# Optimization experiments

Measured on AMD Instinct MI355X. Metric: run time of the kernel, lower is better.

## Reference

```python
import jax, jax.numpy as jnp
import numpy as np
import math

B, LC, LQ, D = 64, 1024, 128, 128


def setup_inputs() -> dict:
    key = jax.random.key(0)
    k1, k2, k3, k4, k5 = jax.random.split(key, 5)
    c_rep = jax.random.normal(k1, (B, LC, D), dtype=jnp.float32)
    q_rep = jax.random.normal(k2, (B, LQ, D), dtype=jnp.float32)
    c_mask = jax.random.randint(k3, (B, LC), 0, 2, dtype=jnp.int32)
    q_mask = jax.random.randint(k4, (B, LQ), 0, 2, dtype=jnp.int32)
    lim = math.sqrt(1.0 / D)
    w = jax.random.uniform(k5, (3 * D,), dtype=jnp.float32, minval=-lim, maxval=lim)
    return {"c_rep": c_rep, "q_rep": q_rep, "c_mask": c_mask, "q_mask": q_mask, "w": w}


def _mask_logits(t, m):
    # mask == 1 means masked (matches original: target*(1-mask) + mask*-1e30)
    return t * (1.0 - m) + m * (-1e30)


def reference(c_rep, q_rep, c_mask, q_mask, w):
    d = c_rep.shape[-1]
    w1, w2, w3 = w[:d], w[d:2 * d], w[2 * d:]
    # Trilinear similarity S[b,i,j] = <ct,w1> + <qt,w2> + <ct*qt,w3>
    # computed without materializing the [B,Lc,Lq,3D] concat tensor.
    S = (c_rep @ w1)[:, :, None] \
        + (q_rep @ w2)[:, None, :] \
        + jnp.einsum('bid,bjd->bij', c_rep * w3, q_rep)  # [B, Lc, Lq]
    qm = q_mask[:, None, :].astype(S.dtype)  # [B, 1, Lq]
    cm = c_mask[:, :, None].astype(S.dtype)  # [B, Lc, 1]
    S1 = jax.nn.softmax(_mask_logits(S, qm), axis=2)  # softmax over query dim
    S2 = jax.nn.softmax(_mask_logits(S, cm), axis=1)  # softmax over context dim
    A = jnp.einsum('bij,bjd->bid', S1, q_rep)  # [B, Lc, D]
    # B_att = S1 @ S2^T @ c_rep, associated right-first to avoid [B,Lc,Lc]
    T = jnp.einsum('bkj,bkd->bjd', S2, c_rep)  # [B, Lq, D]
    B_att = jnp.einsum('bij,bjd->bid', S1, T)  # [B, Lc, D]
    out = jnp.concatenate([c_rep, A, c_rep * A, c_rep * B_att], axis=2)  # [B, Lc, 4D]
    # dropout is identity at inference
    return out
```

## Files before the change

kernel.cpp:

```cpp
#include <hip/hip_runtime.h>
#include <hip/hip_bf16.h>
#include <cstdint>
#include <cstddef>

#define B_   64
#define LC_  1024
#define LQ_  128
#define D_   128

typedef __bf16 bf16;
typedef bf16  bf16x8 __attribute__((ext_vector_type(8)));
typedef bf16  bf16x4 __attribute__((ext_vector_type(4)));
typedef float f32x4  __attribute__((ext_vector_type(4)));

__device__ __forceinline__ f32x4 mfma16(bf16x8 a, bf16x8 b, f32x4 c) {
  return __builtin_amdgcn_mfma_f32_16x16x32_bf16(a, b, c, 0, 0, 0);
}

__global__ __launch_bounds__(256) void k0c(const float* __restrict__ c, const float* __restrict__ w,
                                           float* __restrict__ cw1, bf16* __restrict__ cw3,
                                           bf16* __restrict__ cT) {
  __shared__ float w1s[128];
  __shared__ float w3s[128];
  __shared__ bf16  ctile[128 * 132];
  const int b = blockIdx.y, ks = blockIdx.x;
  const int k0 = ks * 128;
  const int t = threadIdx.x;
  if (t < 128) { w1s[t] = w[t]; w3s[t] = w[256 + t]; }
  __syncthreads();
  {
    const int r = t >> 1, d0 = (t & 1) * 64;
    const float* crow = c + ((size_t)(b * LC_ + k0 + r) * D_ + d0);
    bf16* orow = cw3 + ((size_t)(b * LC_ + k0 + r) * D_ + d0);
    float dot = 0.f;
#pragma unroll
    for (int v = 0; v < 8; ++v) {
      const float4 f0 = ((const float4*)crow)[v * 2 + 0];
      const float4 f1 = ((const float4*)crow)[v * 2 + 1];
      const int dd = d0 + v * 8;
      dot += f0.x * w1s[dd + 0] + f0.y * w1s[dd + 1] + f0.z * w1s[dd + 2] + f0.w * w1s[dd + 3]
           + f1.x * w1s[dd + 4] + f1.y * w1s[dd + 5] + f1.z * w1s[dd + 6] + f1.w * w1s[dd + 7];
      bf16* cr = &ctile[r * 132 + dd];
      cr[0] = (bf16)f0.x; cr[1] = (bf16)f0.y; cr[2] = (bf16)f0.z; cr[3] = (bf16)f0.w;
      cr[4] = (bf16)f1.x; cr[5] = (bf16)f1.y; cr[6] = (bf16)f1.z; cr[7] = (bf16)f1.w;
      bf16x8 o;
      o[0] = (bf16)(f0.x * w3s[dd + 0]); o[1] = (bf16)(f0.y * w3s[dd + 1]);
      o[2] = (bf16)(f0.z * w3s[dd + 2]); o[3] = (bf16)(f0.w * w3s[dd + 3]);
      o[4] = (bf16)(f1.x * w3s[dd + 4]); o[5] = (bf16)(f1.y * w3s[dd + 5]);
      o[6] = (bf16)(f1.z * w3s[dd + 6]); o[7] = (bf16)(f1.w * w3s[dd + 7]);
      *(bf16x8*)(orow + v * 8) = o;
    }
    dot += __shfl_xor(dot, 1);
    if ((t & 1) == 0) cw1[b * LC_ + k0 + r] = dot;
  }
  __syncthreads();
  {
    const int d = t >> 1, kh = (t & 1) * 64;
    bf16* trow = cT + ((size_t)(b * D_ + d) * LC_ + k0 + kh);
#pragma unroll
    for (int v = 0; v < 8; ++v) {
      bf16x8 o;
#pragma unroll
      for (int e = 0; e < 8; ++e) o[e] = ctile[(kh + v * 8 + e) * 132 + d];
      *(bf16x8*)(trow + v * 8) = o;
    }
  }
}

__global__ __launch_bounds__(256) void k0q(const float* __restrict__ q, const float* __restrict__ w,
                                           float* __restrict__ qw2, bf16* __restrict__ qb,
                                           bf16* __restrict__ qT) {
  __shared__ float w2s[128];
  __shared__ bf16  qtile[128 * 132];
  const int b = blockIdx.x;
  const int t = threadIdx.x;
  if (t < 128) w2s[t] = w[128 + t];
  __syncthreads();
  {
    const int r = t >> 1, d0 = (t & 1) * 64;
    const float* qrow = q + ((size_t)(b * LQ_ + r) * D_ + d0);
    bf16* orow = qb + ((size_t)(b * LQ_ + r) * D_ + d0);
    float dot = 0.f;
#pragma unroll
    for (int v = 0; v < 8; ++v) {
      const float4 f0 = ((const float4*)qrow)[v * 2 + 0];
      const float4 f1 = ((const float4*)qrow)[v * 2 + 1];
      const int dd = d0 + v * 8;
      dot += f0.x * w2s[dd + 0] + f0.y * w2s[dd + 1] + f0.z * w2s[dd + 2] + f0.w * w2s[dd + 3]
           + f1.x * w2s[dd + 4] + f1.y * w2s[dd + 5] + f1.z * w2s[dd + 6] + f1.w * w2s[dd + 7];
      bf16x8 o;
      o[0] = (bf16)f0.x; o[1] = (bf16)f0.y; o[2] = (bf16)f0.z; o[3] = (bf16)f0.w;
      o[4] = (bf16)f1.x; o[5] = (bf16)f1.y; o[6] = (bf16)f1.z; o[7] = (bf16)f1.w;
      bf16* qr = &qtile[r * 132 + dd];
#pragma unroll
      for (int e = 0; e < 8; ++e) qr[e] = o[e];
      *(bf16x8*)(orow + v * 8) = o;
    }
    dot += __shfl_xor(dot, 1);
    if ((t & 1) == 0) qw2[b * LQ_ + r] = dot;
  }
  __syncthreads();
  {
    const int d = t >> 1, jh = (t & 1) * 64;
    bf16* trow = qT + ((size_t)(b * D_ + d) * LQ_ + jh);
#pragma unroll
    for (int v = 0; v < 8; ++v) {
      bf16x8 o;
#pragma unroll
      for (int e = 0; e < 8; ++e) o[e] = qtile[(jh + v * 8 + e) * 132 + d];
      *(bf16x8*)(trow + v * 8) = o;
    }
  }
}

__global__ __launch_bounds__(512) void k1p(const float* __restrict__ cw1, const float* __restrict__ qw2,
                                           const int* __restrict__ cmask,
                                           const bf16* __restrict__ cw3, const bf16* __restrict__ cT,
                                           const bf16* __restrict__ qb,
                                           float* __restrict__ Tpart, float* __restrict__ lpart) {
  __shared__ bf16  qs[128 * 136];
  __shared__ bf16  cw3t[64 * 136];
  __shared__ bf16  cTt[128 * 72];
  __shared__ bf16  PT[128 * 72];
  __shared__ float lred[4][128];
  const int ks = blockIdx.x, b = blockIdx.y;
  const int t = threadIdx.x;
  const int w = t >> 6, lane = t & 63, quad = lane >> 4, l15 = lane & 15;
  const int wk = w >> 1, wj = w & 1;

#pragma unroll
  for (int idx = t; idx < 2048; idx += 512) {
    const int row = idx >> 4, ch = idx & 15;
    *(bf16x8*)&qs[row * 136 + ch * 8] =
        *(const bf16x8*)(qb + ((size_t)(b * LQ_ + row) * D_ + ch * 8));
  }
  const f32x4 z = {0.f, 0.f, 0.f, 0.f};
  f32x4 Tacc[4][2];
#pragma unroll
  for (int jt = 0; jt < 4; ++jt) { Tacc[jt][0] = z; Tacc[jt][1] = z; }
  float lacc[4] = {0.f, 0.f, 0.f, 0.f};
  float qv[4];
#pragma unroll
  for (int jt = 0; jt < 4; ++jt) qv[jt] = qw2[b * LQ_ + wj * 64 + jt * 16 + l15];
  __syncthreads();

  for (int kt = 0; kt < 4; ++kt) {
    const int k0g = ks * 256 + kt * 64;
#pragma unroll
    for (int idx = t; idx < 1024; idx += 512) {
      const int row = idx >> 4, ch = idx & 15;
      *(bf16x8*)&cw3t[row * 136 + ch * 8] =
          *(const bf16x8*)(cw3 + ((size_t)(b * LC_ + k0g + row) * D_ + ch * 8));
    }
#pragma unroll
    for (int idx = t; idx < 1024; idx += 512) {
      const int row = idx >> 3, ch = idx & 7;
      *(bf16x8*)&cTt[row * 72 + ch * 8] =
          *(const bf16x8*)(cT + ((size_t)(b * D_ + row) * LC_ + k0g + ch * 8));
    }
    __syncthreads();

    f32x4 S[4] = {z, z, z, z};
#pragma unroll
    for (int kk = 0; kk < 4; ++kk) {
      bf16x8 a = *(bf16x8*)&cw3t[(wk * 16 + l15) * 136 + kk * 32 + quad * 8];
#pragma unroll
      for (int jt = 0; jt < 4; ++jt) {
        bf16x8 bq = *(bf16x8*)&qs[(wj * 64 + jt * 16 + l15) * 136 + kk * 32 + quad * 8];
        S[jt] = mfma16(a, bq, S[jt]);
      }
    }
#pragma unroll
    for (int jt = 0; jt < 4; ++jt) {
      bf16x4 pk;
#pragma unroll
      for (int rr = 0; rr < 4; ++rr) {
        const int krow = k0g + wk * 16 + quad * 4 + rr;
        const float c1 = cw1[b * LC_ + krow];
        const int   cm = cmask[b * LC_ + krow];
        const float p = cm ? 0.f : __expf(S[jt][rr] + c1 + qv[jt]);
        lacc[jt] += p;
        pk[rr] = (bf16)p;
      }
      *(bf16x4*)&PT[(wj * 64 + jt * 16 + l15) * 72 + wk * 16 + quad * 4] = pk;
    }
    __syncthreads();

#pragma unroll
    for (int kk = 0; kk < 2; ++kk) {
      bf16x8 bd0 = *(bf16x8*)&cTt[(wk * 32 + l15) * 72 + kk * 32 + quad * 8];
      bf16x8 bd1 = *(bf16x8*)&cTt[(wk * 32 + 16 + l15) * 72 + kk * 32 + quad * 8];
#pragma unroll
      for (int jt = 0; jt < 4; ++jt) {
        bf16x8 aP = *(bf16x8*)&PT[(wj * 64 + jt * 16 + l15) * 72 + kk * 32 + quad * 8];
        Tacc[jt][0] = mfma16(aP, bd0, Tacc[jt][0]);
        Tacc[jt][1] = mfma16(aP, bd1, Tacc[jt][1]);
      }
    }
    __syncthreads();
  }

#pragma unroll
  for (int jt = 0; jt < 4; ++jt) {
    lacc[jt] += __shfl_xor(lacc[jt], 16);
    lacc[jt] += __shfl_xor(lacc[jt], 32);
  }
  if (lane < 16) {
#pragma unroll
    for (int jt = 0; jt < 4; ++jt) lred[wk][wj * 64 + jt * 16 + l15] = lacc[jt];
  }
  __syncthreads();
  if (t < 128)
    lpart[(size_t)(b * 4 + ks) * 128 + t] =
        lred[0][t] + lred[1][t] + lred[2][t] + lred[3][t];

  float* tp = Tpart + ((size_t)(b * 4 + ks)) * (128 * 128);
#pragma unroll
  for (int jt = 0; jt < 4; ++jt)
#pragma unroll
    for (int dt = 0; dt < 2; ++dt)
#pragma unroll
      for (int rr = 0; rr < 4; ++rr)
        tp[(wj * 64 + jt * 16 + quad * 4 + rr) * 128 + wk * 32 + dt * 16 + l15] =
            Tacc[jt][dt][rr];
}

__global__ __launch_bounds__(256) void k1r(const float* __restrict__ Tpart,
                                           const float* __restrict__ lpart,
                                           bf16* __restrict__ TT) {
  __shared__ float Tsum[32 * 132];
  __shared__ float linv[32];
  const int js = blockIdx.x, b = blockIdx.y;
  const int j0 = js * 32;
  const int t = threadIdx.x;
  const float4* p0 = (const float4*)(Tpart + ((size_t)(b * 4 + 0)) * (128 * 128)) + j0 * 32;
  const float4* p1 = (const float4*)(Tpart + ((size_t)(b * 4 + 1)) * (128 * 128)) + j0 * 32;
  const float4* p2 = (const float4*)(Tpart + ((size_t)(b * 4 + 2)) * (128 * 128)) + j0 * 32;
  const float4* p3 = (const float4*)(Tpart + ((size_t)(b * 4 + 3)) * (128 * 128)) + j0 * 32;
#pragma unroll
  for (int idx = t; idx < 1024; idx += 256) {
    const int row = idx >> 5, seg = idx & 31;
    const float4 v0 = p0[idx];
    const float4 v1 = p1[idx];
    const float4 v2 = p2[idx];
    const float4 v3 = p3[idx];
    float4 s;
    s.x = v0.x + v1.x + v2.x + v3.x;
    s.y = v0.y + v1.y + v2.y + v3.y;
    s.z = v0.z + v1.z + v2.z + v3.z;
    s.w = v0.w + v1.w + v2.w + v3.w;
    *(float4*)&Tsum[row * 132 + seg * 4] = s;
  }
  if (t < 32)
    linv[t] = 1.f / (lpart[(size_t)(b * 4 + 0) * 128 + j0 + t] +
                     lpart[(size_t)(b * 4 + 1) * 128 + j0 + t] +
                     lpart[(size_t)(b * 4 + 2) * 128 + j0 + t] +
                     lpart[(size_t)(b * 4 + 3) * 128 + j0 + t]);
  __syncthreads();
  const int d = t >> 1, jh = (t & 1) * 16;
  bf16x8 o0, o1;
#pragma unroll
  for (int e = 0; e < 8; ++e) {
    o0[e] = (bf16)(Tsum[(jh + e) * 132 + d] * linv[jh + e]);
    o1[e] = (bf16)(Tsum[(jh + 8 + e) * 132 + d] * linv[jh + 8 + e]);
  }
  bf16* dst = TT + ((size_t)(b * D_ + d) * LQ_ + j0 + jh);
  *(bf16x8*)dst = o0;
  *(bf16x8*)(dst + 8) = o1;
}

__global__ __launch_bounds__(256) void k2(const float* __restrict__ c, const float* __restrict__ cw1,
                                          const float* __restrict__ qw2, const int* __restrict__ qmask,
                                          const bf16* __restrict__ cw3, const bf16* __restrict__ qb,
                                          const bf16* __restrict__ qT, const bf16* __restrict__ TT,
                                          float* __restrict__ out) {
  __shared__ __align__(16) char smem[51712];
  bf16* cw3i = (bf16*)(smem);
  bf16* qsl  = (bf16*)(smem + 17408);
  bf16* qTsl = (bf16*)(smem + 26112);
  bf16* TTsl = (bf16*)(smem + 36352);
  bf16* P1   = (bf16*)(smem + 46592);
  float* A32 = (float*)(smem);
  float* B32 = (float*)(smem + 16896);
  const int it = blockIdx.x, b = blockIdx.y;
  const int i0 = it * 64;
  const int t = threadIdx.x;
  const int w = t >> 6, lane = t & 63, quad = lane >> 4, l15 = lane & 15;

#pragma unroll
  for (int idx = t; idx < 1024; idx += 256) {
    const int row = idx >> 4, ch = idx & 15;
    *(bf16x8*)&cw3i[row * 136 + ch * 8] =
        *(const bf16x8*)(cw3 + ((size_t)(b * LC_ + i0 + row) * D_ + ch * 8));
  }
  const f32x4 z = {0.f, 0.f, 0.f, 0.f};
  f32x4 Aacc[8], Bacc[8];
#pragma unroll
  for (int n = 0; n < 8; ++n) { Aacc[n] = z; Bacc[n] = z; }
  float lacc[4] = {0.f, 0.f, 0.f, 0.f};
  __syncthreads();

  for (int jt = 0; jt < 4; ++jt) {
    const int j0 = jt * 32;
#pragma unroll
    for (int idx = t; idx < 512; idx += 256) {
      const int row = idx >> 4, ch = idx & 15;
      *(bf16x8*)&qsl[row * 136 + ch * 8] =
          *(const bf16x8*)(qb + ((size_t)(b * LQ_ + j0 + row) * D_ + ch * 8));
    }
#pragma unroll
    for (int idx = t; idx < 512; idx += 256) {
      const int row = idx >> 2, ch = idx & 3;
      *(bf16x8*)&qTsl[row * 40 + ch * 8] =
          *(const bf16x8*)(qT + ((size_t)(b * D_ + row) * LQ_ + j0 + ch * 8));
    }
#pragma unroll
    for (int idx = t; idx < 512; idx += 256) {
      const int row = idx >> 2, ch = idx & 3;
      *(bf16x8*)&TTsl[row * 40 + ch * 8] =
          *(const bf16x8*)(TT + ((size_t)(b * D_ + row) * LQ_ + j0 + ch * 8));
    }
    __syncthreads();

    f32x4 S0 = z, S1 = z;
#pragma unroll
    for (int kk = 0; kk < 4; ++kk) {
      bf16x8 a  = *(bf16x8*)&cw3i[(w * 16 + l15) * 136 + kk * 32 + quad * 8];
      bf16x8 b0 = *(bf16x8*)&qsl[l15 * 136 + kk * 32 + quad * 8];
      bf16x8 b1 = *(bf16x8*)&qsl[(16 + l15) * 136 + kk * 32 + quad * 8];
      S0 = mfma16(a, b0, S0);
      S1 = mfma16(a, b1, S1);
    }
    const float qv0 = qw2[b * LQ_ + j0 + l15];
    const float qv1 = qw2[b * LQ_ + j0 + 16 + l15];
    const int   qm0 = qmask[b * LQ_ + j0 + l15];
    const int   qm1 = qmask[b * LQ_ + j0 + 16 + l15];
#pragma unroll
    for (int rr = 0; rr < 4; ++rr) {
      const int irow = i0 + w * 16 + quad * 4 + rr;
      const float c1 = cw1[b * LC_ + irow];
      const float p0 = qm0 ? 0.f : __expf(S0[rr] + c1 + qv0);
      const float p1 = qm1 ? 0.f : __expf(S1[rr] + c1 + qv1);
      lacc[rr] += p0 + p1;
      P1[(w * 16 + quad * 4 + rr) * 40 + l15] = (bf16)p0;
      P1[(w * 16 + quad * 4 + rr) * 40 + 16 + l15] = (bf16)p1;
    }
    __syncthreads();

    bf16x8 aP = *(bf16x8*)&P1[(w * 16 + l15) * 40 + quad * 8];
#pragma unroll
    for (int nt = 0; nt < 8; ++nt) {
      bf16x8 bq = *(bf16x8*)&qTsl[(nt * 16 + l15) * 40 + quad * 8];
      bf16x8 bt = *(bf16x8*)&TTsl[(nt * 16 + l15) * 40 + quad * 8];
      Aacc[nt] = mfma16(aP, bq, Aacc[nt]);
      Bacc[nt] = mfma16(aP, bt, Bacc[nt]);
    }
    __syncthreads();
  }

#pragma unroll
  for (int rr = 0; rr < 4; ++rr) {
    float v = lacc[rr];
    v += __shfl_xor(v, 1); v += __shfl_xor(v, 2);
    v += __shfl_xor(v, 4); v += __shfl_xor(v, 8);
    lacc[rr] = 1.f / v;
  }

#pragma unroll
  for (int h = 0; h < 2; ++h) {
    if ((w >> 1) == h) {
      const int lrow0 = (w & 1) * 16 + quad * 4;
#pragma unroll
      for (int nt = 0; nt < 8; ++nt)
#pragma unroll
        for (int rr = 0; rr < 4; ++rr) {
          A32[(lrow0 + rr) * 132 + nt * 16 + l15] = Aacc[nt][rr] * lacc[rr];
          B32[(lrow0 + rr) * 132 + nt * 16 + l15] = Bacc[nt][rr] * lacc[rr];
        }
    }
    __syncthreads();
#pragma unroll
    for (int idx = t; idx < 1024; idx += 256) {
      const int lrow = idx >> 5, seg = idx & 31;
      const size_t grow = (size_t)(b * LC_ + i0 + h * 32 + lrow);
      const float4 c4 = ((const float4*)(c + grow * D_))[seg];
      const float4 a4 = *(float4*)&A32[lrow * 132 + seg * 4];
      const float4 b4 = *(float4*)&B32[lrow * 132 + seg * 4];
      float4* ob = (float4*)(out + grow * 512);
      ob[seg] = c4;
      ob[32 + seg] = a4;
      float4 ca; ca.x = c4.x * a4.x; ca.y = c4.y * a4.y; ca.z = c4.z * a4.z; ca.w = c4.w * a4.w;
      ob[64 + seg] = ca;
      float4 cb; cb.x = c4.x * b4.x; cb.y = c4.y * b4.y; cb.z = c4.z * b4.z; cb.w = c4.w * b4.w;
      ob[96 + seg] = cb;
    }
    __syncthreads();
  }
}

extern "C" void kernel_launch(void* const* d_in, const int* in_sizes, int n_in,
                              void* d_out, int out_size, void* d_ws, size_t ws_size,
                              hipStream_t stream) {
  (void)in_sizes; (void)n_in; (void)out_size; (void)ws_size;
  const float* c     = (const float*)d_in[0];
  const float* q     = (const float*)d_in[1];
  const int*   cmask = (const int*)d_in[2];
  const int*   qmask = (const int*)d_in[3];
  const float* w     = (const float*)d_in[4];
  float* out = (float*)d_out;

  char* ws = (char*)d_ws;
  float* cw1 = (float*)(ws + 0);
  float* qw2 = (float*)(ws + 262144);
  bf16*  cw3 = (bf16*)(ws + 294912);
  bf16*  cT  = (bf16*)(ws + 17072128);
  bf16*  qb  = (bf16*)(ws + 33849344);
  bf16*  qT  = (bf16*)(ws + 35946496);
  bf16*  TT  = (bf16*)(ws + 38043648);

  float* Tpart = out;
  float* lpart = out + 4194304;

  k0c<<<dim3(8, 64), 256, 0, stream>>>(c, w, cw1, cw3, cT);
  k0q<<<dim3(64), 256, 0, stream>>>(q, w, qw2, qb, qT);
  k1p<<<dim3(4, 64), 512, 0, stream>>>(cw1, qw2, cmask, cw3, cT, qb, Tpart, lpart);
  k1r<<<dim3(4, 64), 256, 0, stream>>>(Tpart, lpart, TT);
  k2<<<dim3(16, 64), 256, 0, stream>>>(c, cw1, qw2, qmask, cw3, qb, qT, TT, out);
}
```

Before: 237.7 us.

## Split k1p finer and load MFMA operands directly from global memory

k1p now runs on 16x64 blocks of 256 threads. Each block covers a 128-row context slice and a 64-query half, and the 8 partials are then reduced in k1r. The cw3/cT tiles in k1p and the q/qT/TT tiles in k2 are no longer staged through LDS; MFMA fragments are read straight from global memory, and the remaining LDS arrays use XOR swizzling in place of padding. The aim is to raise occupancy and parallelism and to remove LDS copies and barriers, at the cost of more global/L2 traffic, uncoalesced fragment loads, and a larger partial-sum buffer.

After: 265.9 us. 11.9% more time.

```diff
diff --git a/kernel.cpp b/kernel.cpp
--- a/kernel.cpp
+++ b/kernel.cpp
@@ -16,6 +16,8 @@
 __device__ __forceinline__ f32x4 mfma16(bf16x8 a, bf16x8 b, f32x4 c) {
   return __builtin_amdgcn_mfma_f32_16x16x32_bf16(a, b, c, 0, 0, 0);
 }
+
+__device__ __forceinline__ int swz(int row, int elem) { return elem ^ ((row & 7) << 3); }
 
 __global__ __launch_bounds__(256) void k0c(const float* __restrict__ c, const float* __restrict__ w,
                                            float* __restrict__ cw1, bf16* __restrict__ cw3,
@@ -113,26 +115,26 @@
   }
 }
 
-__global__ __launch_bounds__(512) void k1p(const float* __restrict__ cw1, const float* __restrict__ qw2,
+__global__ __launch_bounds__(256) void k1p(const float* __restrict__ cw1, const float* __restrict__ qw2,
                                            const int* __restrict__ cmask,
                                            const bf16* __restrict__ cw3, const bf16* __restrict__ cT,
                                            const bf16* __restrict__ qb,
                                            float* __restrict__ Tpart, float* __restrict__ lpart) {
-  __shared__ bf16  qs[128 * 136];
-  __shared__ bf16  cw3t[64 * 136];
-  __shared__ bf16  cTt[128 * 72];
-  __shared__ bf16  PT[128 * 72];
-  __shared__ float lred[4][128];
-  const int ks = blockIdx.x, b = blockIdx.y;
+  __shared__ bf16  qs[64 * 128];
+  __shared__ bf16  PT[64 * 64];
+  __shared__ float lred[4][64];
+  const int bx = blockIdx.x;
+  const int ks = bx >> 1, jh = bx & 1;
+  const int b = blockIdx.y;
+  const int j0g = jh * 64;
   const int t = threadIdx.x;
-  const int w = t >> 6, lane = t & 63, quad = lane >> 4, l15 = lane & 15;
-  const int wk = w >> 1, wj = w & 1;
-
-#pragma unroll
-  for (int idx = t; idx < 2048; idx += 512) {
+  const int wk = t >> 6, lane = t & 63, quad = lane >> 4, l15 = lane & 15;
+
+#pragma unroll
+  for (int idx = t; idx < 1024; idx += 256) {
     const int row = idx >> 4, ch = idx & 15;
-    *(bf16x8*)&qs[row * 136 + ch * 8] =
-        *(const bf16x8*)(qb + ((size_t)(b * LQ_ + row) * D_ + ch * 8));
+    *(bf16x8*)&qs[row * 128 + swz(row, ch * 8)] =
+        *(const bf16x8*)(qb + ((size_t)(b * LQ_ + j0g + row) * D_ + ch * 8));
   }
   const f32x4 z = {0.f, 0.f, 0.f, 0.f};
   f32x4 Tacc[4][2];
@@ -141,58 +143,55 @@
   float lacc[4] = {0.f, 0.f, 0.f, 0.f};
   float qv[4];
 #pragma unroll
-  for (int jt = 0; jt < 4; ++jt) qv[jt] = qw2[b * LQ_ + wj * 64 + jt * 16 + l15];
-  __syncthreads();
-
-  for (int kt = 0; kt < 4; ++kt) {
-    const int k0g = ks * 256 + kt * 64;
-#pragma unroll
-    for (int idx = t; idx < 1024; idx += 512) {
-      const int row = idx >> 4, ch = idx & 15;
-      *(bf16x8*)&cw3t[row * 136 + ch * 8] =
-          *(const bf16x8*)(cw3 + ((size_t)(b * LC_ + k0g + row) * D_ + ch * 8));
-    }
-#pragma unroll
-    for (int idx = t; idx < 1024; idx += 512) {
-      const int row = idx >> 3, ch = idx & 7;
-      *(bf16x8*)&cTt[row * 72 + ch * 8] =
-          *(const bf16x8*)(cT + ((size_t)(b * D_ + row) * LC_ + k0g + ch * 8));
-    }
-    __syncthreads();
+  for (int jt = 0; jt < 4; ++jt) qv[jt] = qw2[b * LQ_ + j0g + jt * 16 + l15];
+  __syncthreads();
+
+  for (int kt = 0; kt < 2; ++kt) {
+    const int k0g = ks * 128 + kt * 64;
 
     f32x4 S[4] = {z, z, z, z};
 #pragma unroll
     for (int kk = 0; kk < 4; ++kk) {
-      bf16x8 a = *(bf16x8*)&cw3t[(wk * 16 + l15) * 136 + kk * 32 + quad * 8];
+      const bf16x8 a = *(const bf16x8*)(cw3 +
+          ((size_t)(b * LC_ + k0g + wk * 16 + l15) * D_ + kk * 32 + quad * 8));
 #pragma unroll
       for (int jt = 0; jt < 4; ++jt) {
-        bf16x8 bq = *(bf16x8*)&qs[(wj * 64 + jt * 16 + l15) * 136 + kk * 32 + quad * 8];
+        const int jr = jt * 16 + l15;
+        const bf16x8 bq = *(const bf16x8*)&qs[jr * 128 + swz(jr, kk * 32 + quad * 8)];
         S[jt] = mfma16(a, bq, S[jt]);
       }
     }
+    float c1v[4]; int cmv[4];
+#pragma unroll
+    for (int rr = 0; rr < 4; ++rr) {
+      const int krow = k0g + wk * 16 + quad * 4 + rr;
+      c1v[rr] = cw1[b * LC_ + krow];
+      cmv[rr] = cmask[b * LC_ + krow];
+    }
 #pragma unroll
     for (int jt = 0; jt < 4; ++jt) {
       bf16x4 pk;
 #pragma unroll
       for (int rr = 0; rr < 4; ++rr) {
-        const int krow = k0g + wk * 16 + quad * 4 + rr;
-        const float c1 = cw1[b * LC_ + krow];
-        const int   cm = cmask[b * LC_ + krow];
-        const float p = cm ? 0.f : __expf(S[jt][rr] + c1 + qv[jt]);
+        const float p = cmv[rr] ? 0.f : __expf(S[jt][rr] + c1v[rr] + qv[jt]);
         lacc[jt] += p;
         pk[rr] = (bf16)p;
       }
-      *(bf16x4*)&PT[(wj * 64 + jt * 16 + l15) * 72 + wk * 16 + quad * 4] = pk;
+      const int jr = jt * 16 + l15;
+      *(bf16x4*)&PT[jr * 64 + swz(jr, wk * 16 + quad * 4)] = pk;
     }
     __syncthreads();
 
 #pragma unroll
     for (int kk = 0; kk < 2; ++kk) {
-      bf16x8 bd0 = *(bf16x8*)&cTt[(wk * 32 + l15) * 72 + kk * 32 + quad * 8];
-      bf16x8 bd1 = *(bf16x8*)&cTt[(wk * 32 + 16 + l15) * 72 + kk * 32 + quad * 8];
+      const bf16x8 bd0 = *(const bf16x8*)(cT +
+          ((size_t)(b * D_ + wk * 32 + l15) * LC_ + k0g + kk * 32 + quad * 8));
+      const bf16x8 bd1 = *(const bf16x8*)(cT +
+          ((size_t)(b * D_ + wk * 32 + 16 + l15) * LC_ + k0g + kk * 32 + quad * 8));
 #pragma unroll
       for (int jt = 0; jt < 4; ++jt) {
-        bf16x8 aP = *(bf16x8*)&PT[(wj * 64 + jt * 16 + l15) * 72 + kk * 32 + quad * 8];
+        const int jr = jt * 16 + l15;
+        const bf16x8 aP = *(const bf16x8*)&PT[jr * 64 + swz(jr, kk * 32 + quad * 8)];
         Tacc[jt][0] = mfma16(aP, bd0, Tacc[jt][0]);
         Tacc[jt][1] = mfma16(aP, bd1, Tacc[jt][1]);
       }
@@ -207,21 +206,21 @@
   }
   if (lane < 16) {
 #pragma unroll
-    for (int jt = 0; jt < 4; ++jt) lred[wk][wj * 64 + jt * 16 + l15] = lacc[jt];
-  }
-  __syncthreads();
-  if (t < 128)
-    lpart[(size_t)(b * 4 + ks) * 128 + t] =
+    for (int jt = 0; jt < 4; ++jt) lred[wk][jt * 16 + l15] = lacc[jt];
+  }
+  __syncthreads();
+  if (t < 64)
+    lpart[(size_t)(b * 8 + ks) * 128 + j0g + t] =
         lred[0][t] + lred[1][t] + lred[2][t] + lred[3][t];
 
-  float* tp = Tpart + ((size_t)(b * 4 + ks)) * (128 * 128);
+  float* tp = Tpart + ((size_t)(b * 8 + ks)) * (128 * 128);
 #pragma unroll
   for (int jt = 0; jt < 4; ++jt)
 #pragma unroll
     for (int dt = 0; dt < 2; ++dt)
 #pragma unroll
       for (int rr = 0; rr < 4; ++rr)
-        tp[(wj * 64 + jt * 16 + quad * 4 + rr) * 128 + wk * 32 + dt * 16 + l15] =
+        tp[(j0g + jt * 16 + quad * 4 + rr) * 128 + wk * 32 + dt * 16 + l15] =
             Tacc[jt][dt][rr];
 }
 
@@ -233,38 +232,32 @@
   const int js = blockIdx.x, b = blockIdx.y;
   const int j0 = js * 32;
   const int t = threadIdx.x;
-  const float4* p0 = (const float4*)(Tpart + ((size_t)(b * 4 + 0)) * (128 * 128)) + j0 * 32;
-  const float4* p1 = (const float4*)(Tpart + ((size_t)(b * 4 + 1)) * (128 * 128)) + j0 * 32;
-  const float4* p2 = (const float4*)(Tpart + ((size_t)(b * 4 + 2)) * (128 * 128)) + j0 * 32;
-  const float4* p3 = (const float4*)(Tpart + ((size_t)(b * 4 + 3)) * (128 * 128)) + j0 * 32;
 #pragma unroll
   for (int idx = t; idx < 1024; idx += 256) {
     const int row = idx >> 5, seg = idx & 31;
-    const float4 v0 = p0[idx];
-    const float4 v1 = p1[idx];
-    const float4 v2 = p2[idx];
-    const float4 v3 = p3[idx];
-    float4 s;
-    s.x = v0.x + v1.x + v2.x + v3.x;
-    s.y = v0.y + v1.y + v2.y + v3.y;
-    s.z = v0.z + v1.z + v2.z + v3.z;
-    s.w = v0.w + v1.w + v2.w + v3.w;
+    float4 s = {0.f, 0.f, 0.f, 0.f};
+#pragma unroll
+    for (int i = 0; i < 8; ++i) {
+      const float4 v = ((const float4*)(Tpart + ((size_t)(b * 8 + i)) * (128 * 128)) + j0 * 32)[idx];
+      s.x += v.x; s.y += v.y; s.z += v.z; s.w += v.w;
+    }
     *(float4*)&Tsum[row * 132 + seg * 4] = s;
   }
-  if (t < 32)
-    linv[t] = 1.f / (lpart[(size_t)(b * 4 + 0) * 128 + j0 + t] +
-                     lpart[(size_t)(b * 4 + 1) * 128 + j0 + t] +
-                     lpart[(size_t)(b * 4 + 2) * 128 + j0 + t] +
-                     lpart[(size_t)(b * 4 + 3) * 128 + j0 + t]);
-  __syncthreads();
-  const int d = t >> 1, jh = (t & 1) * 16;
+  if (t < 32) {
+    float l = 0.f;
+#pragma unroll
+    for (int i = 0; i < 8; ++i) l += lpart[(size_t)(b * 8 + i) * 128 + j0 + t];
+    linv[t] = 1.f / l;
+  }
+  __syncthreads();
+  const int d = t >> 1, jhh = (t & 1) * 16;
   bf16x8 o0, o1;
 #pragma unroll
   for (int e = 0; e < 8; ++e) {
-    o0[e] = (bf16)(Tsum[(jh + e) * 132 + d] * linv[jh + e]);
-    o1[e] = (bf16)(Tsum[(jh + 8 + e) * 132 + d] * linv[jh + 8 + e]);
-  }
-  bf16* dst = TT + ((size_t)(b * D_ + d) * LQ_ + j0 + jh);
+    o0[e] = (bf16)(Tsum[(jhh + e) * 132 + d] * linv[jhh + e]);
+    o1[e] = (bf16)(Tsum[(jhh + 8 + e) * 132 + d] * linv[jhh + 8 + e]);
+  }
+  bf16* dst = TT + ((size_t)(b * D_ + d) * LQ_ + j0 + jhh);
   *(bf16x8*)dst = o0;
   *(bf16x8*)(dst + 8) = o1;
 }
@@ -274,12 +267,8 @@
                                           const bf16* __restrict__ cw3, const bf16* __restrict__ qb,
                                           const bf16* __restrict__ qT, const bf16* __restrict__ TT,
                                           float* __restrict__ out) {
-  __shared__ __align__(16) char smem[51712];
-  bf16* cw3i = (bf16*)(smem);
-  bf16* qsl  = (bf16*)(smem + 17408);
-  bf16* qTsl = (bf16*)(smem + 26112);
-  bf16* TTsl = (bf16*)(smem + 36352);
-  bf16* P1   = (bf16*)(smem + 46592);
+  __shared__ __align__(16) char smem[33792];
+  bf16* P1   = (bf16*)(smem);
   float* A32 = (float*)(smem);
   float* B32 = (float*)(smem + 16896);
   const int it = blockIdx.x, b = blockIdx.y;
@@ -287,49 +276,29 @@
   const int t = threadIdx.x;
   const int w = t >> 6, lane = t & 63, quad = lane >> 4, l15 = lane & 15;
 
-#pragma unroll
-  for (int idx = t; idx < 1024; idx += 256) {
-    const int row = idx >> 4, ch = idx & 15;
-    *(bf16x8*)&cw3i[row * 136 + ch * 8] =
-        *(const bf16x8*)(cw3 + ((size_t)(b * LC_ + i0 + row) * D_ + ch * 8));
-  }
+  bf16x8 aF[4];
+#pragma unroll
+  for (int kk = 0; kk < 4; ++kk)
+    aF[kk] = *(const bf16x8*)(cw3 +
+        ((size_t)(b * LC_ + i0 + w * 16 + l15) * D_ + kk * 32 + quad * 8));
+
   const f32x4 z = {0.f, 0.f, 0.f, 0.f};
   f32x4 Aacc[8], Bacc[8];
 #pragma unroll
   for (int n = 0; n < 8; ++n) { Aacc[n] = z; Bacc[n] = z; }
   float lacc[4] = {0.f, 0.f, 0.f, 0.f};
-  __syncthreads();
 
   for (int jt = 0; jt < 4; ++jt) {
     const int j0 = jt * 32;
-#pragma unroll
-    for (int idx = t; idx < 512; idx += 256) {
-      const int row = idx >> 4, ch = idx & 15;
-      *(bf16x8*)&qsl[row * 136 + ch * 8] =
-          *(const bf16x8*)(qb + ((size_t)(b * LQ_ + j0 + row) * D_ + ch * 8));
-    }
-#pragma unroll
-    for (int idx = t; idx < 512; idx += 256) {
-      const int row = idx >> 2, ch = idx & 3;
-      *(bf16x8*)&qTsl[row * 40 + ch * 8] =
-          *(const bf16x8*)(qT + ((size_t)(b * D_ + row) * LQ_ + j0 + ch * 8));
-    }
-#pragma unroll
-    for (int idx = t; idx < 512; idx += 256) {
-      const int row = idx >> 2, ch = idx & 3;
-      *(bf16x8*)&TTsl[row * 40 + ch * 8] =
-          *(const bf16x8*)(TT + ((size_t)(b * D_ + row) * LQ_ + j0 + ch * 8));
-    }
-    __syncthreads();
-
     f32x4 S0 = z, S1 = z;
 #pragma unroll
     for (int kk = 0; kk < 4; ++kk) {
-      bf16x8 a  = *(bf16x8*)&cw3i[(w * 16 + l15) * 136 + kk * 32 + quad * 8];
-      bf16x8 b0 = *(bf16x8*)&qsl[l15 * 136 + kk * 32 + quad * 8];
-      bf16x8 b1 = *(bf16x8*)&qsl[(16 + l15) * 136 + kk * 32 + quad * 8];
-      S0 = mfma16(a, b0, S0);
-      S1 = mfma16(a, b1, S1);
+      const bf16x8 b0 = *(const bf16x8*)(qb +
+          ((size_t)(b * LQ_ + j0 + l15) * D_ + kk * 32 + quad * 8));
+      const bf16x8 b1 = *(const bf16x8*)(qb +
+          ((size_t)(b * LQ_ + j0 + 16 + l15) * D_ + kk * 32 + quad * 8));
+      S0 = mfma16(aF[kk], b0, S0);
+      S1 = mfma16(aF[kk], b1, S1);
     }
     const float qv0 = qw2[b * LQ_ + j0 + l15];
     const float qv1 = qw2[b * LQ_ + j0 + 16 + l15];
@@ -347,11 +316,13 @@
     }
     __syncthreads();
 
-    bf16x8 aP = *(bf16x8*)&P1[(w * 16 + l15) * 40 + quad * 8];
+    const bf16x8 aP = *(bf16x8*)&P1[(w * 16 + l15) * 40 + quad * 8];
 #pragma unroll
     for (int nt = 0; nt < 8; ++nt) {
-      bf16x8 bq = *(bf16x8*)&qTsl[(nt * 16 + l15) * 40 + quad * 8];
-      bf16x8 bt = *(bf16x8*)&TTsl[(nt * 16 + l15) * 40 + quad * 8];
+      const bf16x8 bq = *(const bf16x8*)(qT +
+          ((size_t)(b * D_ + nt * 16 + l15) * LQ_ + j0 + quad * 8));
+      const bf16x8 bt = *(const bf16x8*)(TT +
+          ((size_t)(b * D_ + nt * 16 + l15) * LQ_ + j0 + quad * 8));
       Aacc[nt] = mfma16(aP, bq, Aacc[nt]);
       Bacc[nt] = mfma16(aP, bt, Bacc[nt]);
     }
@@ -419,11 +390,11 @@
   bf16*  TT  = (bf16*)(ws + 38043648);
 
   float* Tpart = out;
-  float* lpart = out + 4194304;
+  float* lpart = out + 8388608;
 
   k0c<<<dim3(8, 64), 256, 0, stream>>>(c, w, cw1, cw3, cT);
   k0q<<<dim3(64), 256, 0, stream>>>(q, w, qw2, qb, qT);
-  k1p<<<dim3(4, 64), 512, 0, stream>>>(cw1, qw2, cmask, cw3, cT, qb, Tpart, lpart);
+  k1p<<<dim3(16, 64), 256, 0, stream>>>(cw1, qw2, cmask, cw3, cT, qb, Tpart, lpart);
   k1r<<<dim3(4, 64), 256, 0, stream>>>(Tpart, lpart, TT);
   k2<<<dim3(16, 64), 256, 0, stream>>>(c, cw1, qw2, qmask, cw3, qb, qT, TT, out);
 }
```
